# Kernel optimization log

Measured on AMD Instinct MI355X. Metric: run time of the kernel, lower is better.

## Reference

```python
import jax, jax.numpy as jnp
import numpy as np

N = 100000   # num_nodes (also in_channels of layer 1, since x=None)
R = 50       # num_relations
B = 30       # num_bases
H = 16       # hidden channels
C = 8        # num_classes
E = 1600000  # num_edges (avg degree 16)


def setup_inputs() -> dict:
    key = jax.random.key(0)
    ks = jax.random.split(key, 10)
    s = 0.05
    edge_index = jax.random.randint(ks[0], (2, E), 0, N, dtype=jnp.int32)
    edge_type = jax.random.randint(ks[1], (E,), 0, R, dtype=jnp.int32)
    # layer 1 (in=N because x is None -> node-index / embedding mode)
    basis1 = jax.random.normal(ks[2], (B, N, H), jnp.float32) * s
    comp1 = jax.random.normal(ks[3], (R, B), jnp.float32) * s
    root1 = jax.random.normal(ks[4], (N, H), jnp.float32) * s
    bias1 = jnp.zeros((H,), jnp.float32)
    # layer 2 (in=H, out=C)
    basis2 = jax.random.normal(ks[5], (B, H, C), jnp.float32) * s
    comp2 = jax.random.normal(ks[6], (R, B), jnp.float32) * s
    root2 = jax.random.normal(ks[7], (H, C), jnp.float32) * s
    bias2 = jnp.zeros((C,), jnp.float32)
    return dict(edge_index=edge_index, edge_type=edge_type,
                basis1=basis1, comp1=comp1, root1=root1, bias1=bias1,
                basis2=basis2, comp2=comp2, root2=root2, bias2=bias2)


def reference(edge_index, edge_type, basis1, comp1, root1, bias1,
              basis2, comp2, root2, bias2):
    src, dst = edge_index[0], edge_index[1]
    # PyG RGCNConv uses aggr='mean' per relation: each message is divided by
    # the number of same-relation incoming edges at its target node.
    seg = dst * R + edge_type                                   # [E] (node, rel) segment id
    cnt = jax.ops.segment_sum(jnp.ones((E,), jnp.float32), seg, num_segments=N * R)
    inv = 1.0 / jnp.maximum(cnt, 1.0)                           # [N*R]
    inv_e = inv[seg][:, None]                                   # [E,1]

    # ---- layer 1: x = None -> message_e = weight[rel_e][src_e] ----
    w1 = jnp.einsum('rb,bnh->rnh', comp1, basis1)               # [R,N,H] basis-combined weights
    msg1 = w1[edge_type, src] * inv_e                           # [E,H]
    h = jax.ops.segment_sum(msg1, dst, num_segments=N)          # [N,H]
    h = h + root1 + bias1                                       # root embedding + bias
    # NOTE: source does `x.relu()` without assignment -> no-op; faithfully omitted.

    # ---- layer 2: mean-aggregate per (node, relation), then per-relation matmul ----
    w2 = jnp.einsum('rb,bhc->rhc', comp2, basis2)               # [R,H,C]
    agg = jax.ops.segment_sum(h[src] * inv_e, seg, num_segments=N * R)
    agg = agg.reshape(N, R, H)                                  # [N,R,H]
    out = jnp.einsum('nrh,rhc->nc', agg, w2) + h @ root2 + bias2
    return out
```

## Files before the change

### kernel.cpp

```cpp
#include <hip/hip_runtime.h>

#define NREL   50
#define NBASE  30
#define HID    16
#define NCLS   8

#define SHIFT   9
#define BWID    (1 << SHIFT)
#define NBUKMAX 512
#define TILE    4096
#define EPB     16
#define W2T     56
#define C1P     36

typedef float    vf4 __attribute__((ext_vector_type(4)));
typedef _Float16 vh8 __attribute__((ext_vector_type(8)));


__global__ void compute_w2_kernel(const float* __restrict__ comp2,
                                  const float* __restrict__ basis2,
                                  float* __restrict__ w2) {
    int i = blockIdx.x * blockDim.x + threadIdx.x;
    if (i >= NREL * HID * NCLS) return;
    int r  = i / (HID * NCLS);
    int hc = i % (HID * NCLS);
    float acc = 0.f;
    #pragma unroll
    for (int b = 0; b < NBASE; ++b)
        acc += comp2[r * NBASE + b] * basis2[b * HID * NCLS + hc];
    w2[i] = acc;
}


__global__ void ghist_kernel(const int* __restrict__ src,
                             const int* __restrict__ dst,
                             int* __restrict__ hs, int* __restrict__ hd,
                             int E, int nbuk) {
    __shared__ int lhs[NBUKMAX], lhd[NBUKMAX];
    for (int j = threadIdx.x; j < nbuk; j += blockDim.x) { lhs[j] = 0; lhd[j] = 0; }
    __syncthreads();
    for (long e = (long)blockIdx.x * blockDim.x + threadIdx.x; e < E;
         e += (long)gridDim.x * blockDim.x) {
        atomicAdd(&lhs[src[e] >> SHIFT], 1);
        atomicAdd(&lhd[dst[e] >> SHIFT], 1);
    }
    __syncthreads();
    for (int j = threadIdx.x; j < nbuk; j += blockDim.x) {
        if (lhs[j]) atomicAdd(&hs[j], lhs[j]);
        if (lhd[j]) atomicAdd(&hd[j], lhd[j]);
    }
}

__global__ void scanbuk_kernel(const int* __restrict__ hs, const int* __restrict__ hd,
                               int* __restrict__ gcs, int* __restrict__ bases_s,
                               int* __restrict__ based, int* __restrict__ gcd,
                               int nbuk, int E) {
    __shared__ int a[NBUKMAX], b[NBUKMAX];
    int tid = threadIdx.x;
    for (int j = tid; j < nbuk; j += blockDim.x) { a[j] = hs[j]; b[j] = hd[j]; }
    __syncthreads();
    if (tid == 0) {
        int run = 0;
        for (int i = 0; i < nbuk; ++i) { int v = a[i]; a[i] = run; run += v; }
        run = 0;
        for (int i = 0; i < nbuk; ++i) { int v = b[i]; b[i] = run; run += v; }
    }
    __syncthreads();
    for (int j = tid; j < nbuk; j += blockDim.x) {
        gcs[j] = a[j]; bases_s[j] = a[j];
        based[j] = b[j]; gcd[j] = b[j];
    }
    if (tid == 0) { bases_s[nbuk] = E; based[nbuk] = E; }
}

__global__ void pass1_kernel(const int* __restrict__ src,
                             const int* __restrict__ dst,
                             const int* __restrict__ et,
                             int* __restrict__ gcur,
                             int* __restrict__ Ax0, int* __restrict__ Ad0, int E) {
    __shared__ int lhist[NBUKMAX], lbase[NBUKMAX], lcur[NBUKMAX];
    int tid = threadIdx.x;
    for (int j = tid; j < NBUKMAX; j += 256) { lhist[j] = 0; lcur[j] = 0; }
    __syncthreads();
    int px[EPB], pd[EPB]; int bk[EPB];
    long e0 = (long)blockIdx.x * TILE;
    #pragma unroll
    for (int j = 0; j < EPB; ++j) {
        long e = e0 + j * 256 + tid;
        if (e < E) {
            int s = src[e], d = dst[e], t = et[e];
            px[j] = s | (t << 17);
            pd[j] = d;
            bk[j] = s >> SHIFT;
            atomicAdd(&lhist[bk[j]], 1);
        } else bk[j] = -1;
    }
    __syncthreads();
    for (int j = tid; j < NBUKMAX; j += 256)
        if (lhist[j] > 0) lbase[j] = atomicAdd(&gcur[j], lhist[j]);
    __syncthreads();
    #pragma unroll
    for (int j = 0; j < EPB; ++j) {
        if (bk[j] >= 0) {
            int r = atomicAdd(&lcur[bk[j]], 1);
            int pos = lbase[bk[j]] + r;
            Ax0[pos] = px[j];
            Ad0[pos] = pd[j];
        }
    }
}

__global__ void pass1b_kernel(const int* __restrict__ Ax0,
                              const int* __restrict__ Ad0,
                              const int* __restrict__ bases_s,
                              int* __restrict__ Ax, int* __restrict__ Ad,
                              int* __restrict__ rowptr_s, int N, int E) {
    __shared__ int lh[BWID], sA[BWID], sB[BWID];
    int blk = blockIdx.x, tid = threadIdx.x;
    int k0 = bases_s[blk], k1 = bases_s[blk + 1], cnt = k1 - k0;
    for (int j = tid; j < BWID; j += 256) lh[j] = 0;
    __syncthreads();
    for (int i = tid; i < cnt; i += 256) {
        int slow = Ax0[k0 + i] & (BWID - 1);
        atomicAdd(&lh[slow], 1);
    }
    __syncthreads();
    for (int j = tid; j < BWID; j += 256) sA[j] = lh[j];
    __syncthreads();
    int* cur = sA; int* oth = sB;
    for (int off = 1; off < BWID; off <<= 1) {
        for (int j = tid; j < BWID; j += 256)
            oth[j] = cur[j] + (j >= off ? cur[j - off] : 0);
        __syncthreads();
        int* t_ = cur; cur = oth; oth = t_;
    }
    for (int j = tid; j < BWID; j += 256) {
        int excl = cur[j] - lh[j];
        oth[j] = excl;
        int s = blk * BWID + j;
        if (s < N) rowptr_s[s] = k0 + excl;
    }
    __syncthreads();
    for (int i = tid; i < cnt; i += 256) {
        int x = Ax0[k0 + i], d = Ad0[k0 + i];
        int slow = x & (BWID - 1);
        int pos = atomicAdd(&oth[slow], 1);
        Ax[k0 + pos] = x;
        Ad[k0 + pos] = d;
    }
    if (blk == 0 && tid == 0) rowptr_s[N] = E;
}

__global__ void pass2_kernel(const int* __restrict__ Ax,
                             const int* __restrict__ Ad,
                             int* __restrict__ gcur, int2* __restrict__ B, int E) {
    __shared__ int lhist[NBUKMAX], lbase[NBUKMAX], lcur[NBUKMAX];
    int tid = threadIdx.x;
    for (int j = tid; j < NBUKMAX; j += 256) { lhist[j] = 0; lcur[j] = 0; }
    __syncthreads();
    int2 p[EPB]; int bk[EPB];
    long e0 = (long)blockIdx.x * TILE;
    #pragma unroll
    for (int j = 0; j < EPB; ++j) {
        long e = e0 + j * 256 + tid;
        if (e < E) {
            int x = Ax[e];
            int d = Ad[e];
            p[j] = make_int2(x, (int)e | ((d & (BWID - 1)) << 21));
            bk[j] = d >> SHIFT;
            atomicAdd(&lhist[bk[j]], 1);
        } else bk[j] = -1;
    }
    __syncthreads();
    for (int j = tid; j < NBUKMAX; j += 256)
        if (lhist[j] > 0) lbase[j] = atomicAdd(&gcur[j], lhist[j]);
    __syncthreads();
    #pragma unroll
    for (int j = 0; j < EPB; ++j) {
        if (bk[j] >= 0) {
            int r = atomicAdd(&lcur[bk[j]], 1);
            B[lbase[bk[j]] + r] = p[j];
        }
    }
}

__global__ void pass3_kernel(const int2* __restrict__ B,
                             const int* __restrict__ based,
                             int2* __restrict__ e2, int* __restrict__ rowptr,
                             int N, int E) {
    __shared__ int lh[BWID], sA[BWID], sB[BWID];
    int blk = blockIdx.x, tid = threadIdx.x;
    int k0 = based[blk], k1 = based[blk + 1], cnt = k1 - k0;
    for (int j = tid; j < BWID; j += 256) lh[j] = 0;
    __syncthreads();
    for (int i = tid; i < cnt; i += 256) {
        int dlow = ((unsigned)B[k0 + i].y) >> 21;
        atomicAdd(&lh[dlow], 1);
    }
    __syncthreads();
    for (int j = tid; j < BWID; j += 256) sA[j] = lh[j];
    __syncthreads();
    int* cur = sA; int* oth = sB;
    for (int off = 1; off < BWID; off <<= 1) {
        for (int j = tid; j < BWID; j += 256)
            oth[j] = cur[j] + (j >= off ? cur[j - off] : 0);
        __syncthreads();
        int* t_ = cur; cur = oth; oth = t_;
    }
    for (int j = tid; j < BWID; j += 256) {
        int excl = cur[j] - lh[j];
        oth[j] = excl;
        int d = blk * BWID + j;
        if (d < N) rowptr[d] = k0 + excl;
    }
    __syncthreads();
    for (int i = tid; i < cnt; i += 256) {
        int2 b = B[k0 + i];
        int dlow = ((unsigned)b.y) >> 21;
        int pos = atomicAdd(&oth[dlow], 1);
        e2[k0 + pos] = make_int2(b.x, b.y & 0x1FFFFF);
    }
    if (blk == 0 && tid == 0) rowptr[N] = E;
}

__global__ void layer1A_node_kernel(const int* __restrict__ Ax,
                                    const int* __restrict__ rowptr_s,
                                    const float* __restrict__ comp1,
                                    const float* __restrict__ basis1,
                                    _Float16* __restrict__ msg, int N) {
    __shared__ float c1s[NREL * C1P];
    for (int i = threadIdx.x; i < NREL * C1P; i += blockDim.x) {
        int t = i / C1P, b = i % C1P;
        c1s[i] = (b < NBASE) ? comp1[t * NBASE + b] : 0.f;
    }
    __syncthreads();
    int gid = threadIdx.x >> 4;
    int l   = threadIdx.x & 15;
    int s = blockIdx.x * 16 + gid;
    if (s >= N) return;
    int k0 = rowptr_s[s], k1 = rowptr_s[s + 1];
    if (k0 == k1) return;

    vf4 b4[8];
    {
        long stride = (long)N * HID;
        const float* bp = basis1 + (long)s * HID + l;
        float breg[32];
        #pragma unroll
        for (int b = 0; b < NBASE; ++b)
            breg[b] = bp[(long)b * stride];
        #pragma unroll
        for (int b = NBASE; b < 32; ++b) breg[b] = 0.f;
        #pragma unroll
        for (int i = 0; i < 8; ++i)
            b4[i] = (vf4){breg[4*i], breg[4*i+1], breg[4*i+2], breg[4*i+3]};
    }

    int k = k0;
    if (k + 4 <= k1) {
        int c0x = Ax[k + 0], c1x = Ax[k + 1], c2x = Ax[k + 2], c3x = Ax[k + 3];
        for (;;) {
            bool more = (k + 8 <= k1);
            int n0, n1, n2, n3;
            if (more) {
                n0 = Ax[k + 4]; n1 = Ax[k + 5]; n2 = Ax[k + 6]; n3 = Ax[k + 7];
            }
            const vf4* c0 = reinterpret_cast<const vf4*>(c1s + (((unsigned)c0x) >> 17) * C1P);
            const vf4* c1 = reinterpret_cast<const vf4*>(c1s + (((unsigned)c1x) >> 17) * C1P);
            const vf4* c2 = reinterpret_cast<const vf4*>(c1s + (((unsigned)c2x) >> 17) * C1P);
            const vf4* c3 = reinterpret_cast<const vf4*>(c1s + (((unsigned)c3x) >> 17) * C1P);
            vf4 a0 = {0.f,0.f,0.f,0.f}, a1 = a0, a2 = a0, a3 = a0;
            #pragma unroll
            for (int i = 0; i < 8; ++i) {
                a0 += c0[i] * b4[i];
                a1 += c1[i] * b4[i];
                a2 += c2[i] * b4[i];
                a3 += c3[i] * b4[i];
            }
            float r0 = (a0.x + a0.y) + (a0.z + a0.w);
            float r1 = (a1.x + a1.y) + (a1.z + a1.w);
            float r2 = (a2.x + a2.y) + (a2.z + a2.w);
            float r3 = (a3.x + a3.y) + (a3.z + a3.w);
            __builtin_nontemporal_store((_Float16)r0, &msg[(long)(k + 0) * HID + l]);
            __builtin_nontemporal_store((_Float16)r1, &msg[(long)(k + 1) * HID + l]);
            __builtin_nontemporal_store((_Float16)r2, &msg[(long)(k + 2) * HID + l]);
            __builtin_nontemporal_store((_Float16)r3, &msg[(long)(k + 3) * HID + l]);
            k += 4;
            if (!more) break;
            c0x = n0; c1x = n1; c2x = n2; c3x = n3;
        }
    }
    for (; k < k1; ++k) {
        int t = ((unsigned)Ax[k]) >> 17;
        const vf4* cr4 = reinterpret_cast<const vf4*>(c1s + t * C1P);
        vf4 acc4 = {0.f, 0.f, 0.f, 0.f};
        #pragma unroll
        for (int i = 0; i < 8; ++i)
            acc4 += cr4[i] * b4[i];
        float acc = (acc4.x + acc4.y) + (acc4.z + acc4.w);
        __builtin_nontemporal_store((_Float16)acc, &msg[(long)k * HID + l]);
    }
}

__global__ void layer1B_kernel(const int2* __restrict__ e2,
                               const int* __restrict__ rowptr,
                               const _Float16* __restrict__ msg,
                               const float* __restrict__ root1,
                               const float* __restrict__ bias1,
                               _Float16* __restrict__ h, float* __restrict__ sinv, int N) {
    long gid = (long)blockIdx.x * blockDim.x + threadIdx.x;
    int d = (int)(gid >> 3);
    if (d >= N) return;
    int q = (int)(gid & 7);
    int k0 = rowptr[d], k1 = rowptr[d + 1];

    float acc[HID];
    #pragma unroll
    for (int i = 0; i < HID; ++i) acc[i] = 0.f;

    for (int k = k0 + q; k < k1; k += 8) {
        int2 v = e2[k];
        unsigned t = ((unsigned)v.x) >> 17;
        int c = 0;
        for (int j = k0; j < k1; ++j)
            c += ((((unsigned)e2[j].x) >> 17) == t);
        float inv = 1.0f / (float)c;
        sinv[k] = inv;
        const vh8* m8 = reinterpret_cast<const vh8*>(msg + (long)v.y * HID);
        vh8 m0 = __builtin_nontemporal_load(m8);
        vh8 m1 = __builtin_nontemporal_load(m8 + 1);
        #pragma unroll
        for (int i = 0; i < 8; ++i) {
            acc[i]     += inv * (float)m0[i];
            acc[i + 8] += inv * (float)m1[i];
        }
    }

    #pragma unroll
    for (int i = 0; i < HID; ++i) {
        acc[i] += __shfl_xor(acc[i], 1);
        acc[i] += __shfl_xor(acc[i], 2);
        acc[i] += __shfl_xor(acc[i], 4);
    }

    if (q == 0) {
        vh8 o0, o1;
        #pragma unroll
        for (int i = 0; i < 8; ++i) {
            o0[i] = (_Float16)(acc[i]     + root1[(size_t)d * HID + i]     + bias1[i]);
            o1[i] = (_Float16)(acc[i + 8] + root1[(size_t)d * HID + i + 8] + bias1[i + 8]);
        }
        vh8* h8 = reinterpret_cast<vh8*>(h + (size_t)d * HID);
        h8[0] = o0;
        h8[1] = o1;
    }
}

__global__ void layer2_kernel(const int2* __restrict__ e2,
                              const int* __restrict__ rowptr,
                              const float* __restrict__ sinv,
                              const float* __restrict__ w2,
                              const _Float16* __restrict__ h,
                              const float* __restrict__ root2,
                              const float* __restrict__ bias2,
                              float* __restrict__ out, int N) {
    __shared__ float w2s[HID * NCLS * W2T];
    for (int i = threadIdx.x; i < NREL * HID * NCLS; i += blockDim.x) {
        int t = i / (HID * NCLS);
        int hc = i % (HID * NCLS);
        w2s[hc * W2T + t] = w2[i];
    }
    __syncthreads();

    long gid = (long)blockIdx.x * blockDim.x + threadIdx.x;
    int d = (int)(gid >> 3);
    if (d >= N) return;
    int q = (int)(gid & 7);
    int k0 = rowptr[d], k1 = rowptr[d + 1];

    float acc[NCLS];
    #pragma unroll
    for (int c = 0; c < NCLS; ++c) acc[c] = 0.f;

    for (int k = k0 + q; k < k1; k += 8) {
        int2 v = e2[k];
        int s = v.x & 0x1FFFF;
        int t = ((unsigned)v.x) >> 17;
        float inv = sinv[k];
        const vh8* h8 = reinterpret_cast<const vh8*>(h + (size_t)s * HID);
        vh8 m0 = h8[0];
        vh8 m1 = h8[1];
        float hv[HID];
        #pragma unroll
        for (int i = 0; i < 8; ++i) { hv[i] = (float)m0[i]; hv[i + 8] = (float)m1[i]; }
        float tmp[NCLS];
        #pragma unroll
        for (int c = 0; c < NCLS; ++c) tmp[c] = 0.f;
        #pragma unroll
        for (int i = 0; i < HID; ++i) {
            #pragma unroll
            for (int c = 0; c < NCLS; ++c)
                tmp[c] += hv[i] * w2s[(i * NCLS + c) * W2T + t];
        }
        #pragma unroll
        for (int c = 0; c < NCLS; ++c) acc[c] += inv * tmp[c];
    }

    #pragma unroll
    for (int c = 0; c < NCLS; ++c) {
        acc[c] += __shfl_xor(acc[c], 1);
        acc[c] += __shfl_xor(acc[c], 2);
        acc[c] += __shfl_xor(acc[c], 4);
    }

    if (q == 0) {
        const vh8* h8 = reinterpret_cast<const vh8*>(h + (size_t)d * HID);
        vh8 m0 = h8[0];
        vh8 m1 = h8[1];
        float hv[HID];
        #pragma unroll
        for (int i = 0; i < 8; ++i) { hv[i] = (float)m0[i]; hv[i + 8] = (float)m1[i]; }
        #pragma unroll
        for (int i = 0; i < HID; ++i) {
            #pragma unroll
            for (int c = 0; c < NCLS; ++c)
                acc[c] += hv[i] * root2[i * NCLS + c];
        }
        #pragma unroll
        for (int c = 0; c < NCLS; ++c) acc[c] += bias2[c];
        float4* o4 = reinterpret_cast<float4*>(out + (size_t)d * NCLS);
        o4[0] = make_float4(acc[0], acc[1], acc[2], acc[3]);
        o4[1] = make_float4(acc[4], acc[5], acc[6], acc[7]);
    }
}


extern "C" void kernel_launch(void* const* d_in, const int* in_sizes, int n_in,
                              void* d_out, int out_size, void* d_ws, size_t ws_size,
                              hipStream_t stream) {
    const int*   edge_index = (const int*)  d_in[0];
    const int*   edge_type  = (const int*)  d_in[1];
    const float* basis1     = (const float*)d_in[2];
    const float* comp1      = (const float*)d_in[3];
    const float* root1      = (const float*)d_in[4];
    const float* bias1      = (const float*)d_in[5];
    const float* basis2     = (const float*)d_in[6];
    const float* comp2      = (const float*)d_in[7];
    const float* root2      = (const float*)d_in[8];
    const float* bias2      = (const float*)d_in[9];
    float* out = (float*)d_out;

    const int E = in_sizes[1];
    const int N = in_sizes[4] / HID;
    const int nbuk = (N + BWID - 1) >> SHIFT;
    const int* src = edge_index;
    const int* dst = edge_index + E;

    char* base = (char*)d_ws;
    size_t off = 0;
    auto alloc = [&](size_t bytes, size_t align) -> char* {
        off = (off + align - 1) & ~(align - 1);
        char* p = base + off;
        off += bytes;
        return p;
    };
    int*  hs       = (int*)  alloc((size_t)NBUKMAX * 4, 4);
    int*  hd       = (int*)  alloc((size_t)NBUKMAX * 4, 4);
    int*  gcs      = (int*)  alloc((size_t)NBUKMAX * 4, 4);
    int*  gcd      = (int*)  alloc((size_t)NBUKMAX * 4, 4);
    int*  bases_s  = (int*)  alloc((size_t)(NBUKMAX + 1) * 4, 4);
    int*  based    = (int*)  alloc((size_t)(NBUKMAX + 1) * 4, 4);
    int*  rowptr   = (int*)  alloc((size_t)(N + 1) * 4, 4);
    int*  rowptr_s = (int*)  alloc((size_t)(N + 1) * 4, 4);
    float* w2      = (float*)alloc((size_t)NREL * HID * NCLS * 4, 16);
    _Float16* h    = (_Float16*)alloc((size_t)N * HID * 2, 16);
    float* sinv    = (float*)alloc((size_t)E * 4, 4);
    int*  Ax0      = (int*)  alloc((size_t)E * 4, 4);
    int*  Ad0      = (int*)  alloc((size_t)E * 4, 4);
    int*  Ax       = (int*)  alloc((size_t)E * 4, 4);
    int*  Ad       = (int*)  alloc((size_t)E * 4, 4);
    int2* B        = (int2*) alloc((size_t)E * 8, 8);
    int2* e2       = (int2*) alloc((size_t)E * 8, 8);
    _Float16* msg  = (_Float16*)alloc((size_t)E * HID * 2, 16);

    hipMemsetAsync(hs, 0, (size_t)NBUKMAX * 2 * 4, stream);

    {   int M = NREL * HID * NCLS;
        compute_w2_kernel<<<(M + 255) / 256, 256, 0, stream>>>(comp2, basis2, w2);
    }
    ghist_kernel<<<2048, 256, 0, stream>>>(src, dst, hs, hd, E, nbuk);
    scanbuk_kernel<<<1, 256, 0, stream>>>(hs, hd, gcs, bases_s, based, gcd, nbuk, E);

    int nblk = (E + TILE - 1) / TILE;
    pass1_kernel<<<nblk, 256, 0, stream>>>(src, dst, edge_type, gcs, Ax0, Ad0, E);
    pass1b_kernel<<<nbuk, 256, 0, stream>>>(Ax0, Ad0, bases_s, Ax, Ad, rowptr_s, N, E);
    pass2_kernel<<<nblk, 256, 0, stream>>>(Ax, Ad, gcd, B, E);
    pass3_kernel<<<nbuk, 256, 0, stream>>>(B, based, e2, rowptr, N, E);

    {   int blocks = (int)((N + 15) / 16);
        layer1A_node_kernel<<<blocks, 256, 0, stream>>>(
            Ax, rowptr_s, comp1, basis1, msg, N);
    }
    {   long total = (long)N * 8;
        layer1B_kernel<<<(int)((total + 255) / 256), 256, 0, stream>>>(
            e2, rowptr, msg, root1, bias1, h, sinv, N);
    }
    {   long total = (long)N * 8;
        layer2_kernel<<<(int)((total + 255) / 256), 256, 0, stream>>>(
            e2, rowptr, sinv, w2, h, root2, bias2, out, N);
    }
}
```

Baseline: 377.2 us.

## Compute layer-1 per-edge messages with f16 MFMA instead of scalar FMAs

Rewrites the layer-1 message kernel so each wavefront handles one source node and computes 16 edges at a time with a 16x16x32 f16 MFMA. The comp1 rows sit in LDS as f16 and the node's 30 basis values are packed into a B fragment. This replaces the per-lane vector FMA dot products and moves from 16 nodes per block to 4. It adds f16 rounding of comp1 and basis1, wastes MFMA rows when a node has fewer than 16 edges, and launches four times as many blocks.

```diff
diff --git a/kernel.cpp b/kernel.cpp
--- a/kernel.cpp
+++ b/kernel.cpp
@@ -11,7 +11,6 @@
 #define TILE    4096
 #define EPB     16
 #define W2T     56
-#define C1P     36
 
 typedef float    vf4 __attribute__((ext_vector_type(4)));
 typedef _Float16 vh8 __attribute__((ext_vector_type(8)));
@@ -223,82 +222,48 @@
     if (blk == 0 && tid == 0) rowptr[N] = E;
 }
 
-__global__ void layer1A_node_kernel(const int* __restrict__ Ax,
+__global__ void layer1A_mfma_kernel(const int* __restrict__ Ax,
                                     const int* __restrict__ rowptr_s,
                                     const float* __restrict__ comp1,
                                     const float* __restrict__ basis1,
                                     _Float16* __restrict__ msg, int N) {
-    __shared__ float c1s[NREL * C1P];
-    for (int i = threadIdx.x; i < NREL * C1P; i += blockDim.x) {
-        int t = i / C1P, b = i % C1P;
-        c1s[i] = (b < NBASE) ? comp1[t * NBASE + b] : 0.f;
-    }
-    __syncthreads();
-    int gid = threadIdx.x >> 4;
-    int l   = threadIdx.x & 15;
-    int s = blockIdx.x * 16 + gid;
+    __shared__ __align__(16) _Float16 c1h[NREL * 32];
+    for (int i = threadIdx.x; i < NREL * 32; i += blockDim.x) {
+        int t = i >> 5, b = i & 31;
+        c1h[i] = (b < NBASE) ? (_Float16)comp1[t * NBASE + b] : (_Float16)0.f;
+    }
+    __syncthreads();
+
+    int wid  = threadIdx.x >> 6;
+    int lane = threadIdx.x & 63;
+    int q  = lane >> 4;
+    int ch = lane & 15;
+    int s = blockIdx.x * 4 + wid;
     if (s >= N) return;
     int k0 = rowptr_s[s], k1 = rowptr_s[s + 1];
     if (k0 == k1) return;
 
-    vf4 b4[8];
-    {
-        long stride = (long)N * HID;
-        const float* bp = basis1 + (long)s * HID + l;
-        float breg[32];
-        #pragma unroll
-        for (int b = 0; b < NBASE; ++b)
-            breg[b] = bp[(long)b * stride];
-        #pragma unroll
-        for (int b = NBASE; b < 32; ++b) breg[b] = 0.f;
-        #pragma unroll
-        for (int i = 0; i < 8; ++i)
-            b4[i] = (vf4){breg[4*i], breg[4*i+1], breg[4*i+2], breg[4*i+3]};
-    }
-
-    int k = k0;
-    if (k + 4 <= k1) {
-        int c0x = Ax[k + 0], c1x = Ax[k + 1], c2x = Ax[k + 2], c3x = Ax[k + 3];
-        for (;;) {
-            bool more = (k + 8 <= k1);
-            int n0, n1, n2, n3;
-            if (more) {
-                n0 = Ax[k + 4]; n1 = Ax[k + 5]; n2 = Ax[k + 6]; n3 = Ax[k + 7];
-            }
-            const vf4* c0 = reinterpret_cast<const vf4*>(c1s + (((unsigned)c0x) >> 17) * C1P);
-            const vf4* c1 = reinterpret_cast<const vf4*>(c1s + (((unsigned)c1x) >> 17) * C1P);
-            const vf4* c2 = reinterpret_cast<const vf4*>(c1s + (((unsigned)c2x) >> 17) * C1P);
-            const vf4* c3 = reinterpret_cast<const vf4*>(c1s + (((unsigned)c3x) >> 17) * C1P);
-            vf4 a0 = {0.f,0.f,0.f,0.f}, a1 = a0, a2 = a0, a3 = a0;
-            #pragma unroll
-            for (int i = 0; i < 8; ++i) {
-                a0 += c0[i] * b4[i];
-                a1 += c1[i] * b4[i];
-                a2 += c2[i] * b4[i];
-                a3 += c3[i] * b4[i];
-            }
-            float r0 = (a0.x + a0.y) + (a0.z + a0.w);
-            float r1 = (a1.x + a1.y) + (a1.z + a1.w);
-            float r2 = (a2.x + a2.y) + (a2.z + a2.w);
-            float r3 = (a3.x + a3.y) + (a3.z + a3.w);
-            __builtin_nontemporal_store((_Float16)r0, &msg[(long)(k + 0) * HID + l]);
-            __builtin_nontemporal_store((_Float16)r1, &msg[(long)(k + 1) * HID + l]);
-            __builtin_nontemporal_store((_Float16)r2, &msg[(long)(k + 2) * HID + l]);
-            __builtin_nontemporal_store((_Float16)r3, &msg[(long)(k + 3) * HID + l]);
-            k += 4;
-            if (!more) break;
-            c0x = n0; c1x = n1; c2x = n2; c3x = n3;
-        }
-    }
-    for (; k < k1; ++k) {
-        int t = ((unsigned)Ax[k]) >> 17;
-        const vf4* cr4 = reinterpret_cast<const vf4*>(c1s + t * C1P);
-        vf4 acc4 = {0.f, 0.f, 0.f, 0.f};
-        #pragma unroll
-        for (int i = 0; i < 8; ++i)
-            acc4 += cr4[i] * b4[i];
-        float acc = (acc4.x + acc4.y) + (acc4.z + acc4.w);
-        __builtin_nontemporal_store((_Float16)acc, &msg[(long)k * HID + l]);
+    vh8 bfrag;
+    #pragma unroll
+    for (int j = 0; j < 8; ++j) {
+        int b = q * 8 + j;
+        float v = (b < NBASE) ? basis1[((long)b * N + s) * HID + ch] : 0.f;
+        bfrag[j] = (_Float16)v;
+    }
+
+    for (int base = k0; base < k1; base += 16) {
+        int e = base + ch;
+        int ec = (e < k1) ? e : (k1 - 1);
+        int t = ((unsigned)Ax[ec]) >> 17;
+        vh8 afrag = *reinterpret_cast<const vh8*>(c1h + t * 32 + q * 8);
+        vf4 d = {0.f, 0.f, 0.f, 0.f};
+        d = __builtin_amdgcn_mfma_f32_16x16x32_f16(afrag, bfrag, d, 0, 0, 0);
+        #pragma unroll
+        for (int r = 0; r < 4; ++r) {
+            int erow = base + q * 4 + r;
+            if (erow < k1)
+                __builtin_nontemporal_store((_Float16)d[r], &msg[(long)erow * HID + ch]);
+        }
     }
 }
 
@@ -477,7 +442,7 @@
     float* sinv    = (float*)alloc((size_t)E * 4, 4);
     int*  Ax0      = (int*)  alloc((size_t)E * 4, 4);
     int*  Ad0      = (int*)  alloc((size_t)E * 4, 4);
-    int*  Ax       = (int*)  alloc((size_t)E * 4, 4);
+    int*  Ax       = (int*)  alloc((size_t)E * 4, 16);
     int*  Ad       = (int*)  alloc((size_t)E * 4, 4);
     int2* B        = (int2*) alloc((size_t)E * 8, 8);
     int2* e2       = (int2*) alloc((size_t)E * 8, 8);
@@ -497,8 +462,8 @@
     pass2_kernel<<<nblk, 256, 0, stream>>>(Ax, Ad, gcd, B, E);
     pass3_kernel<<<nbuk, 256, 0, stream>>>(B, based, e2, rowptr, N, E);
 
-    {   int blocks = (int)((N + 15) / 16);
-        layer1A_node_kernel<<<blocks, 256, 0, stream>>>(
+    {   int blocks = (N + 3) / 4;
+        layer1A_mfma_kernel<<<blocks, 256, 0, stream>>>(
             Ax, rowptr_s, comp1, basis1, msg, N);
     }
     {   long total = (long)N * 8;
```

New measurement: 399.4 us. 1.06x slower.
